# Optimization experiments

Measured on AMD Instinct MI355X. Metric: run time of the kernel, lower is better.

## Reference

```python
import jax, jax.numpy as jnp
import numpy as np

FEW, BATCH, D, STEPS = 128, 4096, 512, 4


def setup_inputs() -> dict:
    key = jax.random.key(0)
    ks = jax.random.split(key, 6)
    H = 2 * D  # LSTMCell hidden size
    return {
        "support": jax.random.normal(ks[0], (FEW, D), jnp.float32),
        "query": jax.random.normal(ks[1], (BATCH, D), jnp.float32),
        "W_ih": jax.random.normal(ks[2], (4 * H, D), jnp.float32) * (1.0 / np.sqrt(H)),
        "W_hh": jax.random.normal(ks[3], (4 * H, H), jnp.float32) * (1.0 / np.sqrt(H)),
        "b_ih": jax.random.normal(ks[4], (4 * H,), jnp.float32) * 0.01,
        "b_hh": jax.random.normal(ks[5], (4 * H,), jnp.float32) * 0.01,
        "process_step": STEPS,
    }


def reference(support, query, W_ih, W_hh, b_ih, b_hh, process_step):
    # support: (few, d); query: (batch, d); LSTMCell hidden = 2d.
    d = query.shape[1]
    batch = query.shape[0]
    h_r = jnp.zeros((batch, 2 * d), query.dtype)
    c = jnp.zeros((batch, 2 * d), query.dtype)
    h = query
    for _ in range(process_step):
        # PyTorch LSTMCell: gates ordered (i, f, g, o)
        gates = query @ W_ih.T + b_ih + h_r @ W_hh.T + b_hh  # (batch, 8d)
        i, f, g, o = jnp.split(gates, 4, axis=1)
        c = jax.nn.sigmoid(f) * c + jax.nn.sigmoid(i) * jnp.tanh(g)
        h_r_ = jax.nn.sigmoid(o) * jnp.tanh(c)  # (batch, 2d)
        h = query + h_r_[:, :d]  # (batch, d)
        attn = jax.nn.softmax(h @ support.T, axis=1)  # (batch, few)
        r = attn @ support  # (batch, d)
        h_r = jnp.concatenate([h, r], axis=1)  # (batch, 2d)
    return h
```

## Files before the change

kernel.cpp:

```cpp
#include <hip/hip_runtime.h>

#define BATCH 4096
#define DDIM  512
#define FEWN  128
#define LDA1  640
#define GATEN 2048
#define CDIM  512

typedef unsigned short ushort_t;
typedef __attribute__((ext_vector_type(8))) short bf16x8;
typedef __attribute__((ext_vector_type(4))) float f32x4;

__device__ inline ushort_t f2bf(float f) {
  unsigned u = __float_as_uint(f);
  unsigned r = (u + 0x7FFFu + ((u >> 16) & 1u)) >> 16;
  return (ushort_t)r;
}
__device__ inline float bf2f(ushort_t h) { return __uint_as_float((unsigned)h << 16); }
__device__ inline float bf2f_u(unsigned h16) { return __uint_as_float(h16 << 16); }

__device__ inline float sigmoidf(float x) { return 1.f / (1.f + __expf(-x)); }
__device__ inline float tanh_fast(float x) {
  float ax = fabsf(x);
  float t = __expf(-2.f * ax);
  float r = (1.f - t) / (1.f + t);
  return copysignf(r, x);
}

__device__ inline int orig_row(int colp) {
  return ((colp >> 4) & 3) * 1024 + ((colp >> 6) << 4) + (colp & 15);
}

__device__ inline void async_copy16(ushort_t* lds, const ushort_t* g) {
  __builtin_amdgcn_global_load_lds(
      (const __attribute__((address_space(1))) unsigned int*)g,
      (__attribute__((address_space(3))) unsigned int*)lds, 16, 0, 0);
}

__device__ inline void xcd_map(int gx, int gy, int id, int& bx, int& by) {
  if ((gx & 7) == 0) {
    const int cpx = gx >> 3;
    const int x = id & 7, s = id >> 3;
    bx = x * cpx + (s % cpx);
    by = s / cpx;
  } else {
    const int nwg = gx * gy;
    const int qq = nwg >> 3, rr = nwg & 7;
    const int x = id & 7, s = id >> 3;
    const int nid = (x < rr ? x * (qq + 1) : rr * (qq + 1) + (x - rr) * qq) + s;
    bx = nid % gx; by = nid / gx;
  }
}

#define STAGE8(dA, dB, kk)                                                   \
    async_copy16(dA,              gA0 + (kk));                               \
    async_copy16(dA + 512,        gA0 + (size_t)16 * lda + (kk));            \
    async_copy16(dA + 4096,       gA0 + (kk) + 32);                          \
    async_copy16(dA + 4096 + 512, gA0 + (size_t)16 * lda + (kk) + 32);       \
    async_copy16(dB,              gB0 + (kk));                               \
    async_copy16(dB + 512,        gB0 + (size_t)16 * ldb + (kk));            \
    async_copy16(dB + 4096,       gB0 + (kk) + 32);                          \
    async_copy16(dB + 4096 + 512, gB0 + (size_t)16 * ldb + (kk) + 32);

#define KLOOP_DBUF()                                                         \
  const int nIter = K >> 6;                                                  \
  { STAGE8(sA, sB, 0) }                                                      \
  if (nIter > 1) { STAGE8(sA + 8192, sB + 8192, 64) }                        \
  for (int kt = 0; kt < nIter; ++kt) {                                       \
    if (kt + 1 < nIter) asm volatile("s_waitcnt vmcnt(8)" ::: "memory");     \
    else                asm volatile("s_waitcnt vmcnt(0)" ::: "memory");     \
    __builtin_amdgcn_s_barrier();                                            \
    const int cur = (kt & 1) * 8192;                                         \
    _Pragma("unroll")                                                        \
    for (int h = 0; h < 2; ++h) {                                            \
      bf16x8 af[4], bfr[4];                                                  \
      _Pragma("unroll")                                                      \
      for (int mi = 0; mi < 4; ++mi)                                         \
        af[mi] = *(const bf16x8*)&lA[cur + h * 4096 + (wr * 64 + mi * 16 + lr) * 32 + kg * 8]; \
      _Pragma("unroll")                                                      \
      for (int ni = 0; ni < 4; ++ni)                                         \
        bfr[ni] = *(const bf16x8*)&lB[cur + h * 4096 + (wc * 64 + ni * 16 + lr) * 32 + kg * 8]; \
      _Pragma("unroll")                                                      \
      for (int mi = 0; mi < 4; ++mi)                                         \
        _Pragma("unroll")                                                    \
        for (int ni = 0; ni < 4; ++ni)                                       \
          acc[mi][ni] = __builtin_amdgcn_mfma_f32_16x16x32_bf16(af[mi], bfr[ni], acc[mi][ni], 0, 0, 0); \
    }                                                                        \
    __builtin_amdgcn_s_barrier();                                            \
    if (kt + 2 < nIter) {                                                    \
      const int k2 = (kt + 2) << 6;                                          \
      STAGE8(sA + cur, sB + cur, k2)                                         \
    }                                                                        \
  }

#define TILE_COMMON()                                                        \
  __shared__ __align__(16) ushort_t lA[2 * 8192];                            \
  __shared__ __align__(16) ushort_t lB[2 * 8192];                            \
  const int tid = threadIdx.x;                                               \
  const int wid = tid >> 6, lane = tid & 63;                                 \
  const int wr = wid >> 1, wc = wid & 1;                                     \
  const int lr = lane & 15, kg = lane >> 4;                                  \
  const int srow = lane >> 2;                                                \
  const int scol = (lane & 3) * 8;                                           \
  f32x4 acc[4][4] = {};                                                      \
  ushort_t* sA = &lA[wid * 1024];                                            \
  ushort_t* sB = &lB[wid * 1024];

template<int MODE>
__launch_bounds__(256)
__global__ void gemm_fused(const ushort_t* __restrict__ A, const ushort_t* __restrict__ B,
                           const ushort_t* __restrict__ base, ushort_t* __restrict__ c,
                           ushort_t* __restrict__ A1out, ushort_t* __restrict__ A2out,
                           const float* __restrict__ query, float* __restrict__ out,
                           int K, int lda, int ldb) {
  TILE_COMMON()
  int bx, by;
  xcd_map(gridDim.x, gridDim.y, blockIdx.y * gridDim.x + blockIdx.x, bx, by);
  const int m0 = by * 128, n0 = bx * 128;
  const ushort_t* gA0 = A + (size_t)(m0 + wid * 32 + srow) * lda + scol;
  const ushort_t* gB0 = B + (size_t)(n0 + wid * 32 + srow) * ldb + scol;
  KLOOP_DBUF()
  const int jj = ((n0 + wc * 64) >> 6) * 16 + lr;
#pragma unroll
  for (int mi = 0; mi < 4; ++mi) {
#pragma unroll
    for (int r = 0; r < 4; ++r) {
      const int row = m0 + wr * 64 + mi * 16 + kg * 4 + r;
      const uint2 p = *(const uint2*)&base[(size_t)row * GATEN + jj * 4];
      const float g0 = bf2f_u(p.x & 0xFFFFu) + acc[mi][0][r];
      const float g1 = bf2f_u(p.x >> 16)     + acc[mi][1][r];
      const float g2 = bf2f_u(p.y & 0xFFFFu) + acc[mi][2][r];
      const float g3 = bf2f_u(p.y >> 16)     + acc[mi][3][r];
      const float si = sigmoidf(g0);
      const float sf = sigmoidf(g1);
      const float tg = tanh_fast(g2);
      const float so = sigmoidf(g3);
      const size_t ci = (size_t)row * CDIM + jj;
      const float cn = sf * bf2f(c[ci]) + si * tg;
      if (MODE != 2) c[ci] = f2bf(cn);
      const float hr = so * tanh_fast(cn);
      if (MODE == 2) {
        out[(size_t)row * DDIM + jj] = query[(size_t)row * DDIM + jj] + hr;
      } else {
        const ushort_t hi = f2bf(hr);
        const ushort_t lo = f2bf(hr - bf2f(hi));
        A1out[(size_t)row * LDA1 + jj] = hi;
        A2out[(size_t)row * DDIM + jj] = lo;
      }
    }
  }
}

__launch_bounds__(256)
__global__ void gemm_splitk6(const ushort_t* __restrict__ A1, const ushort_t* __restrict__ A2,
                             int lda1, int lda2,
                             const ushort_t* __restrict__ Bc, float* __restrict__ Cf) {
  TILE_COMMON()
  const int seg = blockIdx.x >> 1;
  const int koff = (blockIdx.x & 1) * 256;
  const int m0 = blockIdx.y * 128;
  const ushort_t* A = (seg == 1) ? A2 : A1;
  const int lda = (seg == 1) ? lda2 : lda1;
  const int ldb = 1536;
  const ushort_t* gA0 = A + (size_t)(m0 + wid * 32 + srow) * lda + koff + scol;
  const ushort_t* gB0 = Bc + (size_t)(wid * 32 + srow) * 1536 + seg * 512 + koff + scol;
  const int K = 256;
  KLOOP_DBUF()
#pragma unroll
  for (int mi = 0; mi < 4; ++mi)
#pragma unroll
    for (int ni = 0; ni < 4; ++ni)
#pragma unroll
      for (int r = 0; r < 4; ++r) {
        const int row = m0 + wr * 64 + mi * 16 + kg * 4 + r;
        const int col = wc * 64 + ni * 16 + lr;
        atomicAdd(&Cf[(size_t)row * FEWN + col], acc[mi][ni][r]);
      }
}

__launch_bounds__(256)
__global__ void prologue_mega(const ushort_t* __restrict__ Qcat, const ushort_t* __restrict__ Bcat,
                              const ushort_t* __restrict__ whhRP, const ushort_t* __restrict__ wcomb,
                              float* __restrict__ lgBase, ushort_t* __restrict__ B2,
                              ushort_t* __restrict__ gbase, ushort_t* __restrict__ c,
                              ushort_t* __restrict__ A1out, ushort_t* __restrict__ A2out,
                              const float* __restrict__ b1, const float* __restrict__ b2) {
  TILE_COMMON()
  const int b = blockIdx.x;
  if (b < 192) {
    const int lbx = b % 6, lby = b / 6;
    const int seg = lbx >> 1;
    const int koff = (lbx & 1) * 256;
    const int m0 = lby * 128;
    const ushort_t* A = (seg == 1) ? Qcat + 512 : Qcat;
    const int lda = 1536, ldb = 1536;
    const ushort_t* gA0 = A + (size_t)(m0 + wid * 32 + srow) * lda + koff + scol;
    const ushort_t* gB0 = Bcat + (size_t)(wid * 32 + srow) * 1536 + seg * 512 + koff + scol;
    const int K = 256;
    KLOOP_DBUF()
#pragma unroll
    for (int mi = 0; mi < 4; ++mi)
#pragma unroll
      for (int ni = 0; ni < 4; ++ni)
#pragma unroll
        for (int r = 0; r < 4; ++r) {
          const int row = m0 + wr * 64 + mi * 16 + kg * 4 + r;
          const int col = wc * 64 + ni * 16 + lr;
          atomicAdd(&lgBase[(size_t)row * FEWN + col], acc[mi][ni][r]);
        }
  } else if (b < 208) {
    const int m0 = (b - 192) * 128;
    const int lda = 512, ldb = 1536;
    const ushort_t* gA0 = whhRP + (size_t)(m0 + wid * 32 + srow) * lda + scol;
    const ushort_t* gB0 = Bcat + (size_t)(wid * 32 + srow) * 1536 + scol;
    const int K = 512;
    KLOOP_DBUF()
#pragma unroll
    for (int mi = 0; mi < 4; ++mi)
#pragma unroll
      for (int ni = 0; ni < 4; ++ni)
#pragma unroll
        for (int r = 0; r < 4; ++r) {
          const int row = m0 + wr * 64 + mi * 16 + kg * 4 + r;
          const int col = wc * 64 + ni * 16 + lr;
          B2[(size_t)row * LDA1 + 512 + col] = f2bf(acc[mi][ni][r]);
        }
  } else {
    int bx, by;
    xcd_map(32, 32, b - 208, bx, by);
    const int m0 = by * 128, n0 = bx * 128;
    const int lda = 1536, ldb = 512;
    const ushort_t* gA0 = Qcat + (size_t)(m0 + wid * 32 + srow) * lda + scol;
    const ushort_t* gB0 = wcomb + (size_t)(n0 + wid * 32 + srow) * ldb + scol;
    const int K = 512;
    KLOOP_DBUF()
    if (n0 < 2048) {
      const int jj = ((n0 + wc * 64) >> 6) * 16 + lr;
      const float bi0 = b1[jj]        + b2[jj];
      const float bi2 = b1[2048 + jj] + b2[2048 + jj];
      const float bi3 = b1[3072 + jj] + b2[3072 + jj];
#pragma unroll
      for (int mi = 0; mi < 4; ++mi) {
#pragma unroll
        for (int r = 0; r < 4; ++r) {
          const int row = m0 + wr * 64 + mi * 16 + kg * 4 + r;
          const float si = sigmoidf(acc[mi][0][r] + bi0);
          const float tg = tanh_fast(acc[mi][2][r] + bi2);
          const float so = sigmoidf(acc[mi][3][r] + bi3);
          const float cn = si * tg;
          c[(size_t)row * CDIM + jj] = f2bf(cn);
          const float hr = so * tanh_fast(cn);
          const ushort_t hi = f2bf(hr);
          const ushort_t lo = f2bf(hr - bf2f(hi));
          A1out[(size_t)row * LDA1 + jj] = hi;
          A2out[(size_t)row * DDIM + jj] = lo;
        }
      }
    } else {
      const int jj = ((n0 - 2048 + wc * 64) >> 6) * 16 + lr;
      const float bi0 = b1[jj]        + b2[jj];
      const float bi1 = b1[1024 + jj] + b2[1024 + jj];
      const float bi2 = b1[2048 + jj] + b2[2048 + jj];
      const float bi3 = b1[3072 + jj] + b2[3072 + jj];
#pragma unroll
      for (int mi = 0; mi < 4; ++mi)
#pragma unroll
        for (int r = 0; r < 4; ++r) {
          const int row = m0 + wr * 64 + mi * 16 + kg * 4 + r;
          uint2 p;
          p.x = (unsigned)f2bf(acc[mi][0][r] + bi0) | ((unsigned)f2bf(acc[mi][1][r] + bi1) << 16);
          p.y = (unsigned)f2bf(acc[mi][2][r] + bi2) | ((unsigned)f2bf(acc[mi][3][r] + bi3) << 16);
          *(uint2*)&gbase[(size_t)row * GATEN + jj * 4] = p;
        }
    }
  }
}

__global__ void softmax_kernel(const float* __restrict__ logits, const float* __restrict__ baseL,
                               ushort_t* __restrict__ A1) {
  const int row = blockIdx.x * 4 + (threadIdx.x >> 6);
  const int lane = threadIdx.x & 63;
  const size_t ro = (size_t)row * FEWN;
  const float x0 = logits[ro + lane]      + baseL[ro + lane];
  const float x1 = logits[ro + 64 + lane] + baseL[ro + 64 + lane];
  float m = fmaxf(x0, x1);
#pragma unroll
  for (int s = 32; s > 0; s >>= 1) m = fmaxf(m, __shfl_xor(m, s));
  const float e0 = __expf(x0 - m), e1 = __expf(x1 - m);
  float sum = e0 + e1;
#pragma unroll
  for (int s = 32; s > 0; s >>= 1) sum += __shfl_xor(sum, s);
  const float inv = 1.f / sum;
  A1[(size_t)row * LDA1 + 512 + lane]      = f2bf(e0 * inv);
  A1[(size_t)row * LDA1 + 512 + 64 + lane] = f2bf(e1 * inv);
}

__global__ void setup_all(const float* __restrict__ Wih, const float* __restrict__ Whh,
                          const float* __restrict__ q, const float* __restrict__ s,
                          ushort_t* __restrict__ wcomb, ushort_t* __restrict__ B2,
                          ushort_t* __restrict__ whhRP, ushort_t* __restrict__ Q_cat,
                          ushort_t* __restrict__ B_cat, float4* __restrict__ zbase) {
  const int b = blockIdx.x;
  const int tid = threadIdx.x;
  if (b < 8192) {
    const int idx = b * 256 + tid;
    const int r = idx >> 9, cc = idx & 511;
    ushort_t v;
    if (r < 2048) {
      v = f2bf(Wih[(size_t)orig_row(r) * 512 + cc]);
    } else {
      const int og = orig_row(r - 2048);
      v = f2bf(Wih[(size_t)og * 512 + cc] + Whh[(size_t)og * 1024 + cc]);
    }
    wcomb[idx] = v;
  } else if (b < 16384) {
    const int idx = (b - 8192) * 256 + tid;
    const int r = idx >> 10, k = idx & 1023;
    const ushort_t v = f2bf(Whh[(size_t)orig_row(r) * 1024 + k]);
    if (k < 512) B2[(size_t)r * LDA1 + k] = v;
    else         whhRP[(size_t)r * 512 + (k - 512)] = v;
  } else if (b < 24576) {
    const int idx = (b - 16384) * 256 + tid;
    const int bb = idx >> 9, cc = idx & 511;
    const float v = q[idx];
    const ushort_t hi = f2bf(v);
    const ushort_t lo = f2bf(v - bf2f(hi));
    const size_t ro = (size_t)bb * 1536;
    Q_cat[ro + cc] = hi;
    Q_cat[ro + 512 + cc] = lo;
    Q_cat[ro + 1024 + cc] = hi;
  } else if (b < 24832) {
    const int idx = (b - 24576) * 256 + tid;
    const int n = idx >> 9, cc = idx & 511;
    const float v = s[idx];
    const ushort_t hi = f2bf(v);
    const ushort_t lo = f2bf(v - bf2f(hi));
    const size_t ro = (size_t)n * 1536;
    B_cat[ro + cc] = hi;
    B_cat[ro + 512 + cc] = hi;
    B_cat[ro + 1024 + cc] = lo;
  } else {
    const int idx = (b - 24832) * 256 + tid;
    zbase[idx] = make_float4(0.f, 0.f, 0.f, 0.f);
  }
}

extern "C" void kernel_launch(void* const* d_in, const int* in_sizes, int n_in,
                              void* d_out, int out_size, void* d_ws, size_t ws_size,
                              hipStream_t stream) {
  const float* support = (const float*)d_in[0];
  const float* query   = (const float*)d_in[1];
  const float* W_ih    = (const float*)d_in[2];
  const float* W_hh    = (const float*)d_in[3];
  const float* b_ih    = (const float*)d_in[4];
  const float* b_hh    = (const float*)d_in[5];
  float* out = (float*)d_out;

  char* ws = (char*)d_ws;
  size_t off = 0;
  auto alloc = [&](size_t bytes) { char* p = ws + off; off += (bytes + 255) & ~255ull; return p; };
  ushort_t* gates_baseP = (ushort_t*)alloc((size_t)BATCH * GATEN * 2);
  ushort_t* cbuf        = (ushort_t*)alloc((size_t)BATCH * CDIM * 2);
  ushort_t* A1a         = (ushort_t*)alloc((size_t)BATCH * LDA1 * 2);
  ushort_t* A1b         = (ushort_t*)alloc((size_t)BATCH * LDA1 * 2);
  ushort_t* A2a         = (ushort_t*)alloc((size_t)BATCH * DDIM * 2);
  ushort_t* A2b         = (ushort_t*)alloc((size_t)BATCH * DDIM * 2);
  ushort_t* Q_cat       = (ushort_t*)alloc((size_t)BATCH * 1536 * 2);
  ushort_t* wcomb       = (ushort_t*)alloc((size_t)4096 * 512 * 2);
  ushort_t* B2          = (ushort_t*)alloc((size_t)GATEN * LDA1 * 2);
  ushort_t* whhRP       = (ushort_t*)alloc((size_t)GATEN * 512 * 2);
  ushort_t* B_cat       = (ushort_t*)alloc((size_t)FEWN * 1536 * 2);
  const size_t LOFS = (size_t)BATCH * FEWN;
  float*    logits3     = (float*)   alloc(3 * LOFS * 4);
  float*    lgBase      = (float*)   alloc(LOFS * 4);

  const dim3 blk(256);

  setup_all<<<26880, blk, 0, stream>>>(W_ih, W_hh, query, support,
                                       wcomb, B2, whhRP, Q_cat, B_cat,
                                       (float4*)logits3);

  prologue_mega<<<1232, blk, 0, stream>>>(Q_cat, B_cat, whhRP, wcomb,
                                          lgBase, B2, gates_baseP, cbuf,
                                          A1a, A2a, b_ih, b_hh);

  auto attn_phase = [&](int s, ushort_t* A1, ushort_t* A2) {
    float* lg = logits3 + (size_t)s * LOFS;
    gemm_splitk6<<<dim3(6, 32), blk, 0, stream>>>(A1, A2, LDA1, DDIM, B_cat, lg);
    softmax_kernel<<<BATCH / 4, blk, 0, stream>>>(lg, lgBase, A1);
  };

  attn_phase(0, A1a, A2a);

  gemm_fused<1><<<dim3(16, 32), blk, 0, stream>>>(
      A1a, B2, gates_baseP, cbuf, A1b, A2b, nullptr, nullptr, 640, LDA1, LDA1);
  attn_phase(1, A1b, A2b);

  gemm_fused<1><<<dim3(16, 32), blk, 0, stream>>>(
      A1b, B2, gates_baseP, cbuf, A1a, A2a, nullptr, nullptr, 640, LDA1, LDA1);
  attn_phase(2, A1a, A2a);

  gemm_fused<2><<<dim3(16, 32), blk, 0, stream>>>(
      A1a, B2, gates_baseP, cbuf, nullptr, nullptr, query, out, 640, LDA1, LDA1);
}
```

Before: 172.1 us.

## Single-buffer the B tile in LDS to cut shared memory per block

The K-loop now double-buffers only the A tile, while B uses one LDS buffer that is refilled for the next step right after the compute barrier. This cuts LDS per block from 64KB to 48KB, which could let more blocks stay resident per CU. The cost is that B's global-load latency is covered by only one step of lookahead, and the wait counts are retuned to match. That exposed latency can stall MFMA issue.

```diff
diff --git a/kernel.cpp b/kernel.cpp
--- a/kernel.cpp
+++ b/kernel.cpp
@@ -52,22 +52,37 @@
   }
 }
 
-#define STAGE8(dA, dB, kk)                                                   \
+#define TILE_BS()                                                            \
+  __shared__ __align__(16) ushort_t lA[2 * 8192];                            \
+  __shared__ __align__(16) ushort_t lB[8192];                                \
+  const int tid = threadIdx.x;                                               \
+  const int wid = tid >> 6, lane = tid & 63;                                 \
+  const int wr = wid >> 1, wc = wid & 1;                                     \
+  const int lr = lane & 15, kg = lane >> 4;                                  \
+  const int srow = lane >> 2;                                                \
+  const int scol = (lane & 3) * 8;                                           \
+  f32x4 acc[4][4] = {};                                                      \
+  ushort_t* sA = &lA[wid * 1024];                                            \
+  ushort_t* sB = &lB[wid * 1024];
+
+#define STAGE_A8(dA, kk)                                                     \
     async_copy16(dA,              gA0 + (kk));                               \
     async_copy16(dA + 512,        gA0 + (size_t)16 * lda + (kk));            \
     async_copy16(dA + 4096,       gA0 + (kk) + 32);                          \
-    async_copy16(dA + 4096 + 512, gA0 + (size_t)16 * lda + (kk) + 32);       \
-    async_copy16(dB,              gB0 + (kk));                               \
-    async_copy16(dB + 512,        gB0 + (size_t)16 * ldb + (kk));            \
-    async_copy16(dB + 4096,       gB0 + (kk) + 32);                          \
-    async_copy16(dB + 4096 + 512, gB0 + (size_t)16 * ldb + (kk) + 32);
-
-#define KLOOP_DBUF()                                                         \
+    async_copy16(dA + 4096 + 512, gA0 + (size_t)16 * lda + (kk) + 32);
+#define STAGE_B8(kk)                                                         \
+    async_copy16(sB,              gB0 + (kk));                               \
+    async_copy16(sB + 512,        gB0 + (size_t)16 * ldb + (kk));            \
+    async_copy16(sB + 4096,       gB0 + (kk) + 32);                          \
+    async_copy16(sB + 4096 + 512, gB0 + (size_t)16 * ldb + (kk) + 32);
+
+#define KLOOP_BS()                                                           \
   const int nIter = K >> 6;                                                  \
-  { STAGE8(sA, sB, 0) }                                                      \
-  if (nIter > 1) { STAGE8(sA + 8192, sB + 8192, 64) }                        \
+  { STAGE_A8(sA, 0) }                                                        \
+  { STAGE_B8(0) }                                                            \
+  if (nIter > 1) { STAGE_A8(sA + 8192, 64) }                                 \
   for (int kt = 0; kt < nIter; ++kt) {                                       \
-    if (kt + 1 < nIter) asm volatile("s_waitcnt vmcnt(8)" ::: "memory");     \
+    if (kt + 1 < nIter) asm volatile("s_waitcnt vmcnt(4)" ::: "memory");     \
     else                asm volatile("s_waitcnt vmcnt(0)" ::: "memory");     \
     __builtin_amdgcn_s_barrier();                                            \
     const int cur = (kt & 1) * 8192;                                         \
@@ -79,7 +94,7 @@
         af[mi] = *(const bf16x8*)&lA[cur + h * 4096 + (wr * 64 + mi * 16 + lr) * 32 + kg * 8]; \
       _Pragma("unroll")                                                      \
       for (int ni = 0; ni < 4; ++ni)                                         \
-        bfr[ni] = *(const bf16x8*)&lB[cur + h * 4096 + (wc * 64 + ni * 16 + lr) * 32 + kg * 8]; \
+        bfr[ni] = *(const bf16x8*)&lB[h * 4096 + (wc * 64 + ni * 16 + lr) * 32 + kg * 8]; \
       _Pragma("unroll")                                                      \
       for (int mi = 0; mi < 4; ++mi)                                         \
         _Pragma("unroll")                                                    \
@@ -87,24 +102,9 @@
           acc[mi][ni] = __builtin_amdgcn_mfma_f32_16x16x32_bf16(af[mi], bfr[ni], acc[mi][ni], 0, 0, 0); \
     }                                                                        \
     __builtin_amdgcn_s_barrier();                                            \
-    if (kt + 2 < nIter) {                                                    \
-      const int k2 = (kt + 2) << 6;                                          \
-      STAGE8(sA + cur, sB + cur, k2)                                         \
-    }                                                                        \
+    if (kt + 1 < nIter) { const int k1 = (kt + 1) << 6; STAGE_B8(k1) }       \
+    if (kt + 2 < nIter) { const int k2 = (kt + 2) << 6; STAGE_A8(sA + cur, k2) } \
   }
-
-#define TILE_COMMON()                                                        \
-  __shared__ __align__(16) ushort_t lA[2 * 8192];                            \
-  __shared__ __align__(16) ushort_t lB[2 * 8192];                            \
-  const int tid = threadIdx.x;                                               \
-  const int wid = tid >> 6, lane = tid & 63;                                 \
-  const int wr = wid >> 1, wc = wid & 1;                                     \
-  const int lr = lane & 15, kg = lane >> 4;                                  \
-  const int srow = lane >> 2;                                                \
-  const int scol = (lane & 3) * 8;                                           \
-  f32x4 acc[4][4] = {};                                                      \
-  ushort_t* sA = &lA[wid * 1024];                                            \
-  ushort_t* sB = &lB[wid * 1024];
 
 template<int MODE>
 __launch_bounds__(256)
@@ -113,13 +113,13 @@
                            ushort_t* __restrict__ A1out, ushort_t* __restrict__ A2out,
                            const float* __restrict__ query, float* __restrict__ out,
                            int K, int lda, int ldb) {
-  TILE_COMMON()
+  TILE_BS()
   int bx, by;
   xcd_map(gridDim.x, gridDim.y, blockIdx.y * gridDim.x + blockIdx.x, bx, by);
   const int m0 = by * 128, n0 = bx * 128;
   const ushort_t* gA0 = A + (size_t)(m0 + wid * 32 + srow) * lda + scol;
   const ushort_t* gB0 = B + (size_t)(n0 + wid * 32 + srow) * ldb + scol;
-  KLOOP_DBUF()
+  KLOOP_BS()
   const int jj = ((n0 + wc * 64) >> 6) * 16 + lr;
 #pragma unroll
   for (int mi = 0; mi < 4; ++mi) {
@@ -155,7 +155,7 @@
 __global__ void gemm_splitk6(const ushort_t* __restrict__ A1, const ushort_t* __restrict__ A2,
                              int lda1, int lda2,
                              const ushort_t* __restrict__ Bc, float* __restrict__ Cf) {
-  TILE_COMMON()
+  TILE_BS()
   const int seg = blockIdx.x >> 1;
   const int koff = (blockIdx.x & 1) * 256;
   const int m0 = blockIdx.y * 128;
@@ -165,7 +165,7 @@
   const ushort_t* gA0 = A + (size_t)(m0 + wid * 32 + srow) * lda + koff + scol;
   const ushort_t* gB0 = Bc + (size_t)(wid * 32 + srow) * 1536 + seg * 512 + koff + scol;
   const int K = 256;
-  KLOOP_DBUF()
+  KLOOP_BS()
 #pragma unroll
   for (int mi = 0; mi < 4; ++mi)
 #pragma unroll
@@ -185,7 +185,7 @@
                               ushort_t* __restrict__ gbase, ushort_t* __restrict__ c,
                               ushort_t* __restrict__ A1out, ushort_t* __restrict__ A2out,
                               const float* __restrict__ b1, const float* __restrict__ b2) {
-  TILE_COMMON()
+  TILE_BS()
   const int b = blockIdx.x;
   if (b < 192) {
     const int lbx = b % 6, lby = b / 6;
@@ -197,7 +197,7 @@
     const ushort_t* gA0 = A + (size_t)(m0 + wid * 32 + srow) * lda + koff + scol;
     const ushort_t* gB0 = Bcat + (size_t)(wid * 32 + srow) * 1536 + seg * 512 + koff + scol;
     const int K = 256;
-    KLOOP_DBUF()
+    KLOOP_BS()
 #pragma unroll
     for (int mi = 0; mi < 4; ++mi)
 #pragma unroll
@@ -214,7 +214,7 @@
     const ushort_t* gA0 = whhRP + (size_t)(m0 + wid * 32 + srow) * lda + scol;
     const ushort_t* gB0 = Bcat + (size_t)(wid * 32 + srow) * 1536 + scol;
     const int K = 512;
-    KLOOP_DBUF()
+    KLOOP_BS()
 #pragma unroll
     for (int mi = 0; mi < 4; ++mi)
 #pragma unroll
@@ -233,7 +233,7 @@
     const ushort_t* gA0 = Qcat + (size_t)(m0 + wid * 32 + srow) * lda + scol;
     const ushort_t* gB0 = wcomb + (size_t)(n0 + wid * 32 + srow) * ldb + scol;
     const int K = 512;
-    KLOOP_DBUF()
+    KLOOP_BS()
     if (n0 < 2048) {
       const int jj = ((n0 + wc * 64) >> 6) * 16 + lr;
       const float bi0 = b1[jj]        + b2[jj];
```

New measurement: 171.6 us. About the same (-0.3%).
